# Kernel optimization log

Hardware: AMD Instinct MI355X
Metric: run time of the kernel (lower is better)

## Reference

```python
import jax, jax.numpy as jnp
import numpy as np

# blueprint: (root_input_idx, children) where child >= 0 -> input[child], child < 0 -> hidden[-child-1]
BLUEPRINT = [(0, [0, 1, 2, 3]), (4, [4, 5, 6, 7]), (8, [8, 9, 10, 11]), (12, [12, 13, 14, 15]), (0, [-1, -2, -3, -4])]
B, T, V, E, H, TAGS = 32768, 16, 32000, 32, 64, 64


def setup_inputs() -> dict:
    key = jax.random.key(0)
    ks = jax.random.split(key, 13)
    x = jax.random.randint(ks[0], (B, T), 0, V)  # token ids (never hit pad row V)
    s = jax.random.randint(ks[1], (B,), 1, 5)    # lengths in [1, 4]
    sc = 0.125  # ~1/sqrt(H), matches torch LSTM uniform init scale
    emb = (jax.random.normal(ks[2], (V + 1, E), dtype=jnp.float32) * 0.1).at[V].set(0.0)
    Wih = jax.random.uniform(ks[3], (4 * H, E), minval=-sc, maxval=sc, dtype=jnp.float32)
    Whh = jax.random.uniform(ks[4], (4 * H, H), minval=-sc, maxval=sc, dtype=jnp.float32)
    bih = jax.random.uniform(ks[5], (4 * H,), minval=-sc, maxval=sc, dtype=jnp.float32)
    bhh = jax.random.uniform(ks[6], (4 * H,), minval=-sc, maxval=sc, dtype=jnp.float32)
    h0 = jax.random.uniform(ks[7], (H,), minval=-1.0, maxval=1.0, dtype=jnp.float32)
    c0 = jax.random.uniform(ks[8], (H,), minval=-1.0, maxval=1.0, dtype=jnp.float32)
    Wc = jax.random.uniform(ks[9], (E, H + E), minval=-0.1, maxval=0.1, dtype=jnp.float32)
    bc = jnp.zeros((E,), dtype=jnp.float32)
    Wt = jax.random.uniform(ks[10], (TAGS, E), minval=-0.18, maxval=0.18, dtype=jnp.float32)
    bt = jnp.zeros((TAGS,), dtype=jnp.float32)
    return {"x": x, "s": s, "emb": emb, "Wih": Wih, "Whh": Whh, "bih": bih, "bhh": bhh,
            "h0": h0, "c0": c0, "Wc": Wc, "bc": bc, "Wt": Wt, "bt": bt}


def _lstm_seq(cseq, h0b, c0b, Wih, Whh, b):
    # cseq: [B, L, E] -> outputs [B, L, H]; torch gate order i, f, g, o
    def step(carry, xt):
        h, cc = carry
        g = xt @ Wih.T + h @ Whh.T + b
        i, f, gg, o = jnp.split(g, 4, axis=-1)
        cc = jax.nn.sigmoid(f) * cc + jax.nn.sigmoid(i) * jnp.tanh(gg)
        h = jax.nn.sigmoid(o) * jnp.tanh(cc)
        return (h, cc), h
    _, hs = jax.lax.scan(step, (h0b, c0b), jnp.swapaxes(cseq, 0, 1))
    return jnp.swapaxes(hs, 0, 1)


def reference(x, s, emb, Wih, Whh, bih, bhh, h0, c0, Wc, bc, Wt, bt):
    bsz = x.shape[0]
    inputs = emb[x]  # [B, T, E]
    h0b = jnp.broadcast_to(h0[None, :], (bsz, h0.shape[0]))
    c0b = jnp.broadcast_to(c0[None, :], (bsz, c0.shape[0]))
    b = bih + bhh
    hidden = []
    for root, children in BLUEPRINT:
        r = inputs[:, root]  # [B, E]
        ch = [inputs[:, c] if c >= 0 else hidden[-c - 1] for c in children]
        cseq = jnp.stack(ch, axis=1)  # [B, L, E]
        L = cseq.shape[1]
        o = _lstm_seq(cseq, h0b, c0b, Wih, Whh, b)  # [B, L, H]
        # pack/pad semantics: positions t >= s[b] are zero after pad_packed; relu(0)=0
        mask = (jnp.arange(L)[None, :] < s[:, None]).astype(o.dtype)
        o = jax.nn.relu(o) * mask[..., None]
        last = o[:, -1]  # [B, H] (zero where s[b] < L, matching torch)
        comb = jax.nn.relu(jnp.concatenate([r, last], axis=1) @ Wc.T + bc)  # [B, E]
        hidden.append(comb)
    logits = hidden[-1] @ Wt.T + bt  # [B, TAGS]
    return jax.nn.log_softmax(logits, axis=1)
```

## Files before the change

kernel.cpp:

```cpp
#include <hip/hip_runtime.h>

#define NB 32768
#define NT 16
#define NV 32001
#define NE 32
#define NTAGS 64

typedef __attribute__((ext_vector_type(8))) short short8;
typedef __attribute__((ext_vector_type(4))) float f4;

#define MFMA16(a, b, c) __builtin_amdgcn_mfma_f32_16x16x32_bf16(a, b, c, 0, 0, 0)
#define CFENCE() asm volatile("" ::: "memory")
#define LDSSYNC() asm volatile("s_waitcnt lgkmcnt(0)" ::: "memory")

__device__ __forceinline__ float sigm_(float x) {
    return __builtin_amdgcn_rcpf(1.0f + __expf(-x));
}
__device__ __forceinline__ float tanh2_(float x) {
    float e = __expf(-2.0f * x);
    return fmaf(2.0f, __builtin_amdgcn_rcpf(1.0f + e), -1.0f);
}
__device__ __forceinline__ short f2bf(float x) {
    union { float f; unsigned u; } v; v.f = x;
    unsigned r = v.u + 0x7fffu + ((v.u >> 16) & 1u);
    return (short)(r >> 16);
}

__global__ __launch_bounds__(1024) void classify_prep(
    const int* __restrict__ s, const float* __restrict__ emb,
    const float* __restrict__ Wih, const float* __restrict__ Whh,
    const float* __restrict__ bih, const float* __restrict__ bhh,
    const float* __restrict__ Wc, const float* __restrict__ Wt,
    short* __restrict__ embH, short* __restrict__ wpack, short* __restrict__ wc1,
    short* __restrict__ wc2, short* __restrict__ wth, float* __restrict__ bsum,
    int* __restrict__ cH, int* __restrict__ listH, int* __restrict__ listL) {
    __shared__ int wbH[16], wbL[16];
    const int tid = threadIdx.x, b = blockIdx.x;
    if (b < 32) {
        const int row = b * 1024 + tid;
        const bool heavy = s[row] >= 4;
        unsigned long long mk = __ballot(heavy);
        const int wv = tid >> 6, ln = tid & 63;
        if (ln == 0) wbH[wv] = __popcll(mk);
        __syncthreads();
        if (tid == 0) {
            int tH = 0, tL = 0;
#pragma unroll
            for (int i = 0; i < 16; ++i) {
                int ch = wbH[i];
                wbH[i] = tH; wbL[i] = tL;
                tH += ch; tL += 64 - ch;
            }
            cH[b] = tH;
        }
        __syncthreads();
        unsigned long long ltm = (1ull << ln) - 1ull;
        if (heavy) listH[b * 1024 + wbH[wv] + __popcll(mk & ltm)] = row;
        else       listL[b * 1024 + wbL[wv] + __popcll((~mk) & ltm)] = row;
    }
    for (int i = b * 1024 + tid; i < NV * NE; i += 262144) embH[i] = f2bf(emb[i]);
    if (b == 32) {
        for (int t = tid; t < 18432; t += 1024) {
            int r = t / 72, c = t % 72;
            wpack[t] = f2bf(c < 64 ? Whh[r * 64 + c] : 0.f);
        }
        for (int t = tid; t < 10240; t += 1024) {
            int r = t / 40, c = t % 40;
            wpack[18432 + t] = f2bf(c < 32 ? Wih[r * 32 + c] : 0.f);
        }
        if (tid < 1024) { int r = tid >> 5, c = tid & 31; wc1[tid] = f2bf(Wc[r * 96 + c]); }
        for (int t = tid; t < 2048; t += 1024) {
            int r = t >> 6, c = t & 63;
            wc2[t] = f2bf(Wc[r * 96 + 32 + c]);
        }
        for (int t = tid; t < 2048; t += 1024) {
            int r = t >> 5, c = t & 31;
            wth[t] = f2bf(Wt[r * 32 + c]);
        }
        if (tid < 256) bsum[tid] = bih[tid] + bhh[tid];
    }
}

__global__ __launch_bounds__(256, 2) void main_fused(
    const int* __restrict__ x, const float* __restrict__ emb,
    const float* __restrict__ h0, const float* __restrict__ c0,
    const float* __restrict__ Wc, const float* __restrict__ bc,
    const float* __restrict__ Wt, const float* __restrict__ bt,
    const float* __restrict__ bsum,
    const short* __restrict__ wpack, const short* __restrict__ wc1,
    const short* __restrict__ wc2, const short* __restrict__ wth,
    const short* __restrict__ embH, const int* __restrict__ cH,
    const int* __restrict__ listH, const int* __restrict__ listL,
    float* __restrict__ out) {
    __shared__ __align__(16) short sWhh[18432];
    __shared__ __align__(16) short sHA[4][16 * 72];
    __shared__ __align__(16) short sCmb[4][16 * 40];
    __shared__ __align__(16) short sC4[4][4 * 40];

    const int tid = threadIdx.x, wave = tid >> 6, lane = tid & 63;
    const int q = lane >> 4, n = lane & 15;
    const int NW = gridDim.x * 4;
    const int gw = blockIdx.x * 4 + wave;

    int cs = (lane < 32) ? cH[lane] : 0;
    int v = cs;
#pragma unroll
    for (int o = 1; o < 32; o <<= 1) { int t2 = __shfl_up(v, o); if (lane >= o) v += t2; }
    const int vIncl = v, vExcl = v - cs;
    const int nH = __shfl(vIncl, 31);
    const int nL = NB - nH;
    const int liIncl = (lane + 1) * 1024 - vIncl;
    const int liExcl = lane * 1024 - vExcl;
    const int nHW = (nH + 3) >> 2;

    if ((int)blockIdx.x * 4 < nHW) {
        for (int i = tid; i < 2304; i += 256)
            ((uint4*)sWhh)[i] = ((const uint4*)wpack)[i];
        __syncthreads();
    }

    if (gw < nHW) {
        short* hA = sHA[wave];
        short* cmb = sCmb[wave];
        short* c4 = sC4[wave];
        const short* wihG = wpack + 18432;

        short8 wihR[16];
#pragma unroll
        for (int tl = 0; tl < 16; ++tl)
            wihR[tl] = *(const short8*)&wihG[(tl * 16 + n) * 40 + q * 8];

        float bias16[16];
#pragma unroll
        for (int tl = 0; tl < 16; ++tl) bias16[tl] = bsum[tl * 16 + n];
        float bc2[2] = {bc[n], bc[16 + n]};
        float bt4[4] = {bt[n], bt[16 + n], bt[32 + n], bt[48 + n]};
        float c0v[4]; short h0b[4];
#pragma unroll
        for (int u = 0; u < 4; ++u) { c0v[u] = c0[u * 16 + n]; h0b[u] = f2bf(h0[u * 16 + n]); }

        const f4 zero4 = {0.f, 0.f, 0.f, 0.f};
        f4 acc[16];
        float cst[4][4];

        auto initSt = [&]() {
#pragma unroll
            for (int u = 0; u < 4; ++u) {
                short hb = h0b[u];
#pragma unroll
                for (int r = 0; r < 4; ++r) {
                    cst[r][u] = c0v[u];
                    hA[(q * 4 + r) * 72 + u * 16 + n] = hb;
                }
            }
            CFENCE();
        };
        auto doStep = [&](short8 aP, bool doRelu) {
            short8 ah0 = *(const short8*)&hA[n * 72 + q * 8];
            short8 ah1 = *(const short8*)&hA[n * 72 + 32 + q * 8];
#pragma unroll
            for (int tl = 0; tl < 16; ++tl) acc[tl] = MFMA16(aP, wihR[tl], zero4);
#pragma unroll
            for (int tl = 0; tl < 16; ++tl) {
                const short* rbp = &sWhh[(tl * 16 + n) * 72 + q * 8];
                f4 t0 = acc[tl];
                t0 = MFMA16(ah0, *(const short8*)rbp, t0);
                t0 = MFMA16(ah1, *(const short8*)(rbp + 32), t0);
                acc[tl] = t0;
            }
            CFENCE();
#pragma unroll
            for (int u = 0; u < 4; ++u)
#pragma unroll
                for (int r = 0; r < 4; ++r) {
                    float ip = acc[u][r] + bias16[u];
                    float fp = acc[4 + u][r] + bias16[4 + u];
                    float gp = acc[8 + u][r] + bias16[8 + u];
                    float op = acc[12 + u][r] + bias16[12 + u];
                    float cc = fmaf(sigm_(fp), cst[r][u], sigm_(ip) * tanh2_(gp));
                    cst[r][u] = cc;
                    float hh = sigm_(op) * tanh2_(cc);
                    if (doRelu) hh = fmaxf(hh, 0.f);
                    hA[(q * 4 + r) * 72 + u * 16 + n] = f2bf(hh);
                }
            CFENCE();
        };
        auto combMM = [&](short8 aroot, short* dst, int strideSel) {
            short8 lh0 = *(const short8*)&hA[n * 72 + q * 8];
            short8 lh1 = *(const short8*)&hA[n * 72 + 32 + q * 8];
#pragma unroll
            for (int tl2 = 0; tl2 < 2; ++tl2) {
                float bv = bc2[tl2];
                f4 t0 = {bv, bv, bv, bv};
                short8 b1 = *(const short8*)&wc1[(tl2 * 16 + n) * 32 + q * 8];
                t0 = MFMA16(aroot, b1, t0);
                const short* rbp = &wc2[(tl2 * 16 + n) * 64 + q * 8];
                t0 = MFMA16(lh0, *(const short8*)rbp, t0);
                t0 = MFMA16(lh1, *(const short8*)(rbp + 32), t0);
#pragma unroll
                for (int r = 0; r < 4; ++r) {
                    int ui = strideSel ? (q * 4 + r) : r;
                    dst[ui * 40 + tl2 * 16 + n] = f2bf(fmaxf(t0[r], 0.f));
                }
            }
            CFENCE();
        };

#pragma unroll 1
        for (int it = gw; it * 4 < nH; it += NW) {
            const int base = it * 4;
            int idxq = min(base + q, nH - 1);
            int sl = 0;
#pragma unroll
            for (int b2 = 0; b2 < 32; ++b2) sl += (__shfl(vIncl, b2) <= idxq) ? 1 : 0;
            const int row = listH[sl * 1024 + idxq - __shfl(vExcl, sl)];
            const int tokAll = x[row * 16 + n];
            const int liBase = (n & 3) * 16 + (n >> 2) * 4;

            initSt();
            int tok = __shfl(tokAll, liBase);
            short8 aNext = *(const short8*)&embH[tok * 32 + q * 8];
            const short8 aRoot = aNext;
#pragma unroll 1
            for (int t = 0; t < 4; ++t) {
                short8 aP = aNext;
                if (t < 3) {
                    int tk2 = __shfl(tokAll, liBase + t + 1);
                    aNext = *(const short8*)&embH[tk2 * 32 + q * 8];
                }
                doStep(aP, t == 3);
            }
            combMM(aRoot, cmb, 1);

            initSt();
            int tokR = __shfl(tokAll, (n & 3) * 16);
            short8 aR4 = *(const short8*)&embH[tokR * 32 + q * 8];
#pragma unroll 1
            for (int t = 0; t < 4; ++t) {
                short8 aC = *(const short8*)&cmb[(t * 4 + (n & 3)) * 40 + q * 8];
                doStep(aC, t == 3);
            }
            combMM(aR4, c4, 0);

            short8 cA = *(const short8*)&c4[(n & 3) * 40 + q * 8];
            f4 a3[4];
#pragma unroll
            for (int tl3 = 0; tl3 < 4; ++tl3) {
                float bv = bt4[tl3];
                f4 t0 = {bv, bv, bv, bv};
                short8 bW = *(const short8*)&wth[(tl3 * 16 + n) * 32 + q * 8];
                a3[tl3] = MFMA16(cA, bW, t0);
            }
#pragma unroll
            for (int r = 0; r < 4; ++r) {
                float l0 = a3[0][r], l1 = a3[1][r], l2 = a3[2][r], l3 = a3[3][r];
                float mx = fmaxf(fmaxf(l0, l1), fmaxf(l2, l3));
#pragma unroll
                for (int o2 = 8; o2; o2 >>= 1) mx = fmaxf(mx, __shfl_xor(mx, o2));
                float sm = __expf(l0 - mx) + __expf(l1 - mx) +
                           __expf(l2 - mx) + __expf(l3 - mx);
#pragma unroll
                for (int o2 = 8; o2; o2 >>= 1) sm += __shfl_xor(sm, o2);
                float lse = mx + __logf(sm);
                if (q == r && base + r < nH) {
                    out[row * 64 + n] = l0 - lse;
                    out[row * 64 + 16 + n] = l1 - lse;
                    out[row * 64 + 32 + n] = l2 - lse;
                    out[row * 64 + 48 + n] = l3 - lse;
                }
            }
        }
    }

    if (nL > 0) {
        short* cmbL = sCmb[wave];
        f4 bcV[2], btV[4];
#pragma unroll
        for (int t = 0; t < 2; ++t) { float bv = bc[t * 16 + n]; bcV[t] = f4{bv, bv, bv, bv}; }
#pragma unroll
        for (int t = 0; t < 4; ++t) { float bv = bt[t * 16 + n]; btV[t] = f4{bv, bv, bv, bv}; }
        const int lgw = NW - 1 - gw;
#pragma unroll 1
        for (int base = lgw * 16; base < nL; base += NW * 16) {
            int idx = min(base + lane, nL - 1);
            int sl = 0;
#pragma unroll
            for (int b2 = 0; b2 < 32; ++b2) sl += (__shfl(liIncl, b2) <= idx) ? 1 : 0;
            const int lrow = listL[sl * 1024 + idx - __shfl(liExcl, sl)];
            const int ltok = x[lrow * 16];
            short8 aE = *(const short8*)&embH[__shfl(ltok, n) * 32 + q * 8];
#pragma unroll
            for (int tl2 = 0; tl2 < 2; ++tl2) {
                short8 b1 = *(const short8*)&wc1[(tl2 * 16 + n) * 32 + q * 8];
                f4 t0 = MFMA16(aE, b1, bcV[tl2]);
#pragma unroll
                for (int r = 0; r < 4; ++r)
                    cmbL[(q * 4 + r) * 40 + tl2 * 16 + n] = f2bf(fmaxf(t0[r], 0.f));
            }
            CFENCE();
            short8 cA = *(const short8*)&cmbL[n * 40 + q * 8];
            f4 a3[4];
#pragma unroll
            for (int tl3 = 0; tl3 < 4; ++tl3) {
                short8 bW = *(const short8*)&wth[(tl3 * 16 + n) * 32 + q * 8];
                a3[tl3] = MFMA16(cA, bW, btV[tl3]);
            }
#pragma unroll
            for (int r = 0; r < 4; ++r) {
                float l0 = a3[0][r], l1 = a3[1][r], l2 = a3[2][r], l3 = a3[3][r];
                float mx = fmaxf(fmaxf(l0, l1), fmaxf(l2, l3));
#pragma unroll
                for (int o2 = 8; o2; o2 >>= 1) mx = fmaxf(mx, __shfl_xor(mx, o2));
                float sm = __expf(l0 - mx) + __expf(l1 - mx) +
                           __expf(l2 - mx) + __expf(l3 - mx);
#pragma unroll
                for (int o2 = 8; o2; o2 >>= 1) sm += __shfl_xor(sm, o2);
                float lse = mx + __logf(sm);
                int rowO = __shfl(lrow, q * 4 + r);
                if (base + q * 4 + r < nL) {
                    out[rowO * 64 + n] = l0 - lse;
                    out[rowO * 64 + 16 + n] = l1 - lse;
                    out[rowO * 64 + 32 + n] = l2 - lse;
                    out[rowO * 64 + 48 + n] = l3 - lse;
                }
            }
            CFENCE();
        }
    }
}

__global__ __launch_bounds__(512) void tagger_fallback(
    const int* __restrict__ x, const int* __restrict__ s, const float* __restrict__ emb,
    const float* __restrict__ Wih, const float* __restrict__ Whh,
    const float* __restrict__ bih, const float* __restrict__ bhh,
    const float* __restrict__ h0, const float* __restrict__ c0,
    const float* __restrict__ Wc, const float* __restrict__ bc,
    const float* __restrict__ Wt, const float* __restrict__ bt,
    float* __restrict__ out) {
    __shared__ float4 WhhP[4096];
    __shared__ float combBuf[8][128];
    for (int i = threadIdx.x; i < 4096; i += 512) {
        int k = i & 63, jj = i >> 6;
        WhhP[k * 64 + jj] = make_float4(Whh[jj * 64 + k], Whh[(jj + 64) * 64 + k],
                                        Whh[(jj + 128) * 64 + k], Whh[(jj + 192) * 64 + k]);
    }
    __syncthreads();
    const int wave = threadIdx.x >> 6, j = threadIdx.x & 63, jm = j & 31;
    const int b = blockIdx.x * 8 + wave;
    const int sv = s[b];
    const int* xb = x + b * NT;
    const float bcj = bc[jm];
    auto rc_val = [&](int tok) -> float {
        float r = 0.f;
#pragma unroll
        for (int k = 0; k < 32; ++k) r = fmaf(emb[tok * NE + k], Wc[jm * 96 + k], r);
        return r;
    };
    float comb4;
    if (sv >= 4) {
        const float h0j = h0[j], c0j = c0[j];
        float4 bsj = make_float4(bih[j] + bhh[j], bih[j + 64] + bhh[j + 64],
                                 bih[j + 128] + bhh[j + 128], bih[j + 192] + bhh[j + 192]);
#pragma unroll 1
        for (int node = 0; node < 4; ++node) {
            float h = h0j, c = c0j;
#pragma unroll 1
            for (int t = 0; t < 4; ++t) {
                int tok = xb[node * 4 + t];
                float4 p = bsj;
#pragma unroll
                for (int k = 0; k < 32; ++k) {
                    float e = emb[tok * NE + k];
                    p.x = fmaf(e, Wih[j * 32 + k], p.x);
                    p.y = fmaf(e, Wih[(j + 64) * 32 + k], p.y);
                    p.z = fmaf(e, Wih[(j + 128) * 32 + k], p.z);
                    p.w = fmaf(e, Wih[(j + 192) * 32 + k], p.w);
                }
                float4 a = make_float4(0.f, 0.f, 0.f, 0.f);
#pragma unroll
                for (int k = 0; k < 64; ++k) {
                    float hk = __shfl(h, k);
                    float4 w = WhhP[k * 64 + j];
                    a.x = fmaf(hk, w.x, a.x); a.y = fmaf(hk, w.y, a.y);
                    a.z = fmaf(hk, w.z, a.z); a.w = fmaf(hk, w.w, a.w);
                }
                a.x += p.x; a.y += p.y; a.z += p.z; a.w += p.w;
                float ig = sigm_(a.x), fg = sigm_(a.y), gg = tanh2_(a.z), og = sigm_(a.w);
                c = fmaf(fg, c, ig * gg);
                h = og * tanh2_(c);
            }
            float last = fmaxf(h, 0.f);
            float acc = rc_val(xb[node * 4]) + bcj;
#pragma unroll
            for (int k = 0; k < 64; ++k)
                acc = fmaf(__shfl(last, k), Wc[jm * 96 + 32 + k], acc);
            if (j < 32) combBuf[wave][node * 32 + j] = fmaxf(acc, 0.f);
        }
        LDSSYNC();
        float h = h0j, c = c0j;
#pragma unroll 1
        for (int t = 0; t < 4; ++t) {
            float4 a = make_float4(0.f, 0.f, 0.f, 0.f);
#pragma unroll
            for (int k = 0; k < 32; ++k) {
                float ck = combBuf[wave][t * 32 + k];
                a.x = fmaf(ck, Wih[j * 32 + k], a.x);
                a.y = fmaf(ck, Wih[(j + 64) * 32 + k], a.y);
                a.z = fmaf(ck, Wih[(j + 128) * 32 + k], a.z);
                a.w = fmaf(ck, Wih[(j + 192) * 32 + k], a.w);
            }
#pragma unroll
            for (int k = 0; k < 64; ++k) {
                float hk = __shfl(h, k);
                float4 w = WhhP[k * 64 + j];
                a.x = fmaf(hk, w.x, a.x); a.y = fmaf(hk, w.y, a.y);
                a.z = fmaf(hk, w.z, a.z); a.w = fmaf(hk, w.w, a.w);
            }
            a.x += bih[j] + bhh[j]; a.y += bih[j + 64] + bhh[j + 64];
            a.z += bih[j + 128] + bhh[j + 128]; a.w += bih[j + 192] + bhh[j + 192];
            float ig = sigm_(a.x), fg = sigm_(a.y), gg = tanh2_(a.z), og = sigm_(a.w);
            c = fmaf(fg, c, ig * gg);
            h = og * tanh2_(c);
        }
        float last = fmaxf(h, 0.f);
        float acc = rc_val(xb[0]) + bcj;
#pragma unroll
        for (int k = 0; k < 64; ++k)
            acc = fmaf(__shfl(last, k), Wc[jm * 96 + 32 + k], acc);
        comb4 = fmaxf(acc, 0.f);
    } else {
        comb4 = fmaxf(rc_val(xb[0]) + bcj, 0.f);
    }
    float logit = bt[j];
    const float* wtr = Wt + j * 32;
#pragma unroll
    for (int k = 0; k < 32; ++k) logit = fmaf(__shfl(comb4, k), wtr[k], logit);
    float mx = logit;
#pragma unroll
    for (int off = 32; off; off >>= 1) mx = fmaxf(mx, __shfl_xor(mx, off));
    float ex = __expf(logit - mx);
    float sum = ex;
#pragma unroll
    for (int off = 32; off; off >>= 1) sum += __shfl_xor(sum, off);
    out[b * 64 + j] = logit - mx - __logf(sum);
}

extern "C" void kernel_launch(void* const* d_in, const int* in_sizes, int n_in,
                              void* d_out, int out_size, void* d_ws, size_t ws_size,
                              hipStream_t stream) {
    const int* x = (const int*)d_in[0];
    const int* s = (const int*)d_in[1];
    const float* emb = (const float*)d_in[2];
    const float* Wih = (const float*)d_in[3];
    const float* Whh = (const float*)d_in[4];
    const float* bih = (const float*)d_in[5];
    const float* bhh = (const float*)d_in[6];
    const float* h0 = (const float*)d_in[7];
    const float* c0 = (const float*)d_in[8];
    const float* Wc = (const float*)d_in[9];
    const float* bc = (const float*)d_in[10];
    const float* Wt = (const float*)d_in[11];
    const float* bt = (const float*)d_in[12];
    float* out = (float*)d_out;

    auto al16 = [](size_t v) { return (v + 15) & ~(size_t)15; };
    size_t off = 0;
    size_t oWpack = off; off = al16(off + (size_t)28672 * 2);
    size_t oWc1 = off;   off = al16(off + 1024 * 2);
    size_t oWc2 = off;   off = al16(off + 2048 * 2);
    size_t oWt = off;    off = al16(off + 2048 * 2);
    size_t oBsum = off;  off = al16(off + 256 * 4);
    size_t oEmbH = off;  off = al16(off + (size_t)NV * NE * 2);
    size_t oCH = off;    off = al16(off + 32 * 4);
    size_t oListH = off; off = al16(off + (size_t)NB * 4);
    size_t oListL = off; off = al16(off + (size_t)NB * 4);
    size_t need = off;

    char* ws = (char*)d_ws;
    if (ws_size >= need) {
        short* wpack = (short*)(ws + oWpack);
        short* wc1 = (short*)(ws + oWc1);
        short* wc2 = (short*)(ws + oWc2);
        short* wth = (short*)(ws + oWt);
        float* bsum = (float*)(ws + oBsum);
        short* embH = (short*)(ws + oEmbH);
        int* cHp = (int*)(ws + oCH);
        int* listH = (int*)(ws + oListH);
        int* listL = (int*)(ws + oListL);

        classify_prep<<<dim3(256), dim3(1024), 0, stream>>>(
            s, emb, Wih, Whh, bih, bhh, Wc, Wt,
            embH, wpack, wc1, wc2, wth, bsum, cHp, listH, listL);
        main_fused<<<dim3(768), dim3(256), 0, stream>>>(
            x, emb, h0, c0, Wc, bc, Wt, bt, bsum,
            wpack, wc1, wc2, wth, embH, cHp, listH, listL, out);
    } else {
        tagger_fallback<<<dim3(4096), dim3(512), 0, stream>>>(
            x, s, emb, Wih, Whh, bih, bhh, h0, c0, Wc, bc, Wt, bt, out);
    }
}
```

Measured before the change: 151.2 us.

## Share top-level LSTM across block waves by splitting gates per wave

Heavy rows are now handled per block in groups of 16 instead of per wave in groups of 4. The final-level LSTM over the four combined children is batched across the whole block, with each wave computing one 16-unit gate slice and exchanging hidden state through shared memory under block barriers. This removes the redundant 4x-padded top-level recurrence, in which only 4 of 16 MFMA rows were useful. Light rows are handed to dedicated non-heavy blocks when available, and h0 fragments are kept in registers rather than rewritten to LDS. The cost is added __syncthreads per step, which could stall waves, and a different load split between heavy and light blocks.

```diff
diff --git a/kernel.cpp b/kernel.cpp
--- a/kernel.cpp
+++ b/kernel.cpp
@@ -96,6 +96,7 @@
     __shared__ __align__(16) short sHA[4][16 * 72];
     __shared__ __align__(16) short sCmb[4][16 * 40];
     __shared__ __align__(16) short sC4[4][4 * 40];
+    __shared__ int sRow[16];
 
     const int tid = threadIdx.x, wave = tid >> 6, lane = tid & 63;
     const int q = lane >> 4, n = lane & 15;
@@ -111,18 +112,19 @@
     const int nL = NB - nH;
     const int liIncl = (lane + 1) * 1024 - vIncl;
     const int liExcl = lane * 1024 - vExcl;
-    const int nHW = (nH + 3) >> 2;
-
-    if ((int)blockIdx.x * 4 < nHW) {
+    const int nHB = (nH + 15) >> 4;
+    const bool heavyBlk = (int)blockIdx.x < nHB;
+
+    if (heavyBlk) {
         for (int i = tid; i < 2304; i += 256)
             ((uint4*)sWhh)[i] = ((const uint4*)wpack)[i];
         __syncthreads();
     }
 
-    if (gw < nHW) {
+    if (heavyBlk) {
         short* hA = sHA[wave];
-        short* cmb = sCmb[wave];
-        short* c4 = sC4[wave];
+        short* cmbB = sCmb[0];
+        short* c4 = sC4[0];
         const short* wihG = wpack + 18432;
 
         short8 wihR[16];
@@ -135,29 +137,22 @@
         for (int tl = 0; tl < 16; ++tl) bias16[tl] = bsum[tl * 16 + n];
         float bc2[2] = {bc[n], bc[16 + n]};
         float bt4[4] = {bt[n], bt[16 + n], bt[32 + n], bt[48 + n]};
-        float c0v[4]; short h0b[4];
-#pragma unroll
-        for (int u = 0; u < 4; ++u) { c0v[u] = c0[u * 16 + n]; h0b[u] = f2bf(h0[u * 16 + n]); }
+        float c0v[4];
+#pragma unroll
+        for (int u = 0; u < 4; ++u) c0v[u] = c0[u * 16 + n];
+        short8 h0f0, h0f1;
+#pragma unroll
+        for (int j = 0; j < 8; ++j) {
+            h0f0[j] = f2bf(h0[q * 8 + j]);
+            h0f1[j] = f2bf(h0[32 + q * 8 + j]);
+        }
+        const float c0w = c0[wave * 16 + n];
 
         const f4 zero4 = {0.f, 0.f, 0.f, 0.f};
         f4 acc[16];
         float cst[4][4];
 
-        auto initSt = [&]() {
-#pragma unroll
-            for (int u = 0; u < 4; ++u) {
-                short hb = h0b[u];
-#pragma unroll
-                for (int r = 0; r < 4; ++r) {
-                    cst[r][u] = c0v[u];
-                    hA[(q * 4 + r) * 72 + u * 16 + n] = hb;
-                }
-            }
-            CFENCE();
-        };
-        auto doStep = [&](short8 aP, bool doRelu) {
-            short8 ah0 = *(const short8*)&hA[n * 72 + q * 8];
-            short8 ah1 = *(const short8*)&hA[n * 72 + 32 + q * 8];
+        auto doStep = [&](short8 aP, short8 ah0, short8 ah1, bool doRelu) {
 #pragma unroll
             for (int tl = 0; tl < 16; ++tl) acc[tl] = MFMA16(aP, wihR[tl], zero4);
 #pragma unroll
@@ -185,42 +180,27 @@
                 }
             CFENCE();
         };
-        auto combMM = [&](short8 aroot, short* dst, int strideSel) {
-            short8 lh0 = *(const short8*)&hA[n * 72 + q * 8];
-            short8 lh1 = *(const short8*)&hA[n * 72 + 32 + q * 8];
-#pragma unroll
-            for (int tl2 = 0; tl2 < 2; ++tl2) {
-                float bv = bc2[tl2];
-                f4 t0 = {bv, bv, bv, bv};
-                short8 b1 = *(const short8*)&wc1[(tl2 * 16 + n) * 32 + q * 8];
-                t0 = MFMA16(aroot, b1, t0);
-                const short* rbp = &wc2[(tl2 * 16 + n) * 64 + q * 8];
-                t0 = MFMA16(lh0, *(const short8*)rbp, t0);
-                t0 = MFMA16(lh1, *(const short8*)(rbp + 32), t0);
-#pragma unroll
-                for (int r = 0; r < 4; ++r) {
-                    int ui = strideSel ? (q * 4 + r) : r;
-                    dst[ui * 40 + tl2 * 16 + n] = f2bf(fmaxf(t0[r], 0.f));
-                }
-            }
-            CFENCE();
-        };
 
 #pragma unroll 1
-        for (int it = gw; it * 4 < nH; it += NW) {
-            const int base = it * 4;
-            int idxq = min(base + q, nH - 1);
+        for (int itb = blockIdx.x; itb * 16 < nH; itb += (int)gridDim.x) {
+            const int base = itb * 16;
+            int idxq = min(base + wave * 4 + q, nH - 1);
             int sl = 0;
 #pragma unroll
             for (int b2 = 0; b2 < 32; ++b2) sl += (__shfl(vIncl, b2) <= idxq) ? 1 : 0;
             const int row = listH[sl * 1024 + idxq - __shfl(vExcl, sl)];
+            if (n == 0) sRow[wave * 4 + q] = row;
             const int tokAll = x[row * 16 + n];
             const int liBase = (n & 3) * 16 + (n >> 2) * 4;
 
-            initSt();
+#pragma unroll
+            for (int u = 0; u < 4; ++u)
+#pragma unroll
+                for (int r = 0; r < 4; ++r) cst[r][u] = c0v[u];
             int tok = __shfl(tokAll, liBase);
             short8 aNext = *(const short8*)&embH[tok * 32 + q * 8];
             const short8 aRoot = aNext;
+            short8 a0 = h0f0, a1 = h0f1;
 #pragma unroll 1
             for (int t = 0; t < 4; ++t) {
                 short8 aP = aNext;
@@ -228,103 +208,203 @@
                     int tk2 = __shfl(tokAll, liBase + t + 1);
                     aNext = *(const short8*)&embH[tk2 * 32 + q * 8];
                 }
-                doStep(aP, t == 3);
-            }
-            combMM(aRoot, cmb, 1);
-
-            initSt();
-            int tokR = __shfl(tokAll, (n & 3) * 16);
-            short8 aR4 = *(const short8*)&embH[tokR * 32 + q * 8];
+                doStep(aP, a0, a1, t == 3);
+                if (t < 3) {
+                    a0 = *(const short8*)&hA[n * 72 + q * 8];
+                    a1 = *(const short8*)&hA[n * 72 + 32 + q * 8];
+                }
+            }
+            {
+                short8 lh0 = *(const short8*)&hA[n * 72 + q * 8];
+                short8 lh1 = *(const short8*)&hA[n * 72 + 32 + q * 8];
+#pragma unroll
+                for (int tl2 = 0; tl2 < 2; ++tl2) {
+                    float bv = bc2[tl2];
+                    f4 t0 = {bv, bv, bv, bv};
+                    short8 b1 = *(const short8*)&wc1[(tl2 * 16 + n) * 32 + q * 8];
+                    t0 = MFMA16(aRoot, b1, t0);
+                    const short* rbp = &wc2[(tl2 * 16 + n) * 64 + q * 8];
+                    t0 = MFMA16(lh0, *(const short8*)rbp, t0);
+                    t0 = MFMA16(lh1, *(const short8*)(rbp + 32), t0);
+#pragma unroll
+                    for (int r = 0; r < 4; ++r) {
+                        int m = q * 4 + r;
+                        cmbB[((m >> 2) * 16 + wave * 4 + (m & 3)) * 40 + tl2 * 16 + n] =
+                            f2bf(fmaxf(t0[r], 0.f));
+                    }
+                }
+            }
+            __syncthreads();
+
+            float bias4[4];
+            short8 wih4[4];
+#pragma unroll
+            for (int j = 0; j < 4; ++j) {
+                bias4[j] = bsum[(j * 4 + wave) * 16 + n];
+                wih4[j] = *(const short8*)&wihG[((j * 4 + wave) * 16 + n) * 40 + q * 8];
+            }
+            short8 aCs0 = *(const short8*)&cmbB[(0 * 16 + n) * 40 + q * 8];
+            short8 aCs1 = *(const short8*)&cmbB[(1 * 16 + n) * 40 + q * 8];
+            short8 aCs2 = *(const short8*)&cmbB[(2 * 16 + n) * 40 + q * 8];
+            short8 aCs3 = *(const short8*)&cmbB[(3 * 16 + n) * 40 + q * 8];
+            float cstw[4] = {c0w, c0w, c0w, c0w};
+            short8 b0 = h0f0, b1 = h0f1;
+            f4 ac4[4];
+#pragma unroll
+            for (int t = 0; t < 4; ++t) {
+                short* hbw = (t & 1) ? sHA[1] : sHA[0];
+                short8 aC = (t == 0) ? aCs0 : (t == 1) ? aCs1 : (t == 2) ? aCs2 : aCs3;
+#pragma unroll
+                for (int j = 0; j < 4; ++j) ac4[j] = MFMA16(aC, wih4[j], zero4);
+#pragma unroll
+                for (int j = 0; j < 4; ++j) {
+                    const short* rbp = &sWhh[((j * 4 + wave) * 16 + n) * 72 + q * 8];
+                    f4 t0 = ac4[j];
+                    t0 = MFMA16(b0, *(const short8*)rbp, t0);
+                    t0 = MFMA16(b1, *(const short8*)(rbp + 32), t0);
+                    ac4[j] = t0;
+                }
+                CFENCE();
+#pragma unroll
+                for (int r = 0; r < 4; ++r) {
+                    float ip = ac4[0][r] + bias4[0];
+                    float fp = ac4[1][r] + bias4[1];
+                    float gp = ac4[2][r] + bias4[2];
+                    float op = ac4[3][r] + bias4[3];
+                    float cc = fmaf(sigm_(fp), cstw[r], sigm_(ip) * tanh2_(gp));
+                    cstw[r] = cc;
+                    float hh = sigm_(op) * tanh2_(cc);
+                    if (t == 3) hh = fmaxf(hh, 0.f);
+                    hbw[(q * 4 + r) * 72 + wave * 16 + n] = f2bf(hh);
+                }
+                CFENCE();
+                __syncthreads();
+                if (t < 3) {
+                    b0 = *(const short8*)&hbw[n * 72 + q * 8];
+                    b1 = *(const short8*)&hbw[n * 72 + 32 + q * 8];
+                }
+            }
+
+            {
+                const short* hL = sHA[1];
+                int rv = sRow[n];
+                int tokR = x[rv * 16];
+                short8 aR = *(const short8*)&embH[tokR * 32 + q * 8];
+                short8 lb0 = *(const short8*)&hL[n * 72 + q * 8];
+                short8 lb1 = *(const short8*)&hL[n * 72 + 32 + q * 8];
+#pragma unroll
+                for (int tl2 = 0; tl2 < 2; ++tl2) {
+                    float bv = bc2[tl2];
+                    f4 t0 = {bv, bv, bv, bv};
+                    short8 b1f = *(const short8*)&wc1[(tl2 * 16 + n) * 32 + q * 8];
+                    t0 = MFMA16(aR, b1f, t0);
+                    const short* rbp = &wc2[(tl2 * 16 + n) * 64 + q * 8];
+                    t0 = MFMA16(lb0, *(const short8*)rbp, t0);
+                    t0 = MFMA16(lb1, *(const short8*)(rbp + 32), t0);
+                    if (q == wave) {
+#pragma unroll
+                        for (int r = 0; r < 4; ++r)
+                            c4[(wave * 4 + r) * 40 + tl2 * 16 + n] = f2bf(fmaxf(t0[r], 0.f));
+                    }
+                }
+            }
+            __syncthreads();
+
+            {
+                short8 cA = *(const short8*)&c4[n * 40 + q * 8];
+                f4 a3[4];
+#pragma unroll
+                for (int tl3 = 0; tl3 < 4; ++tl3) {
+                    float bv = bt4[tl3];
+                    f4 t0 = {bv, bv, bv, bv};
+                    short8 bW = *(const short8*)&wth[(tl3 * 16 + n) * 32 + q * 8];
+                    a3[tl3] = MFMA16(cA, bW, t0);
+                }
+#pragma unroll
+                for (int r = 0; r < 4; ++r) {
+                    float l0 = a3[0][r], l1 = a3[1][r], l2 = a3[2][r], l3 = a3[3][r];
+                    float mx = fmaxf(fmaxf(l0, l1), fmaxf(l2, l3));
+#pragma unroll
+                    for (int o2 = 8; o2; o2 >>= 1) mx = fmaxf(mx, __shfl_xor(mx, o2));
+                    float sm = __expf(l0 - mx) + __expf(l1 - mx) +
+                               __expf(l2 - mx) + __expf(l3 - mx);
+#pragma unroll
+                    for (int o2 = 8; o2; o2 >>= 1) sm += __shfl_xor(sm, o2);
+                    float lse = mx + __logf(sm);
+                    if (q == wave && base + wave * 4 + r < nH) {
+                        int ro = sRow[wave * 4 + r];
+                        out[ro * 64 + n] = l0 - lse;
+                        out[ro * 64 + 16 + n] = l1 - lse;
+                        out[ro * 64 + 32 + n] = l2 - lse;
+                        out[ro * 64 + 48 + n] = l3 - lse;
+                    }
+                }
+            }
+        }
+    }
+
+    if (nL > 0) {
+        const int nLB = max((int)gridDim.x - nHB, 0);
+        int lw, nlw;
+        if (nLB > 0) {
+            if (heavyBlk) { lw = -1; nlw = 0; }
+            else { lw = ((int)blockIdx.x - nHB) * 4 + wave; nlw = nLB * 4; }
+        } else {
+            lw = NW - 1 - gw; nlw = NW;
+        }
+        if (lw >= 0) {
+            short* cmbL = sCmb[wave];
+            f4 bcV[2], btV[4];
+#pragma unroll
+            for (int t = 0; t < 2; ++t) { float bv = bc[t * 16 + n]; bcV[t] = f4{bv, bv, bv, bv}; }
+#pragma unroll
+            for (int t = 0; t < 4; ++t) { float bv = bt[t * 16 + n]; btV[t] = f4{bv, bv, bv, bv}; }
 #pragma unroll 1
-            for (int t = 0; t < 4; ++t) {
-                short8 aC = *(const short8*)&cmb[(t * 4 + (n & 3)) * 40 + q * 8];
-                doStep(aC, t == 3);
-            }
-            combMM(aR4, c4, 0);
-
-            short8 cA = *(const short8*)&c4[(n & 3) * 40 + q * 8];
-            f4 a3[4];
-#pragma unroll
-            for (int tl3 = 0; tl3 < 4; ++tl3) {
-                float bv = bt4[tl3];
-                f4 t0 = {bv, bv, bv, bv};
-                short8 bW = *(const short8*)&wth[(tl3 * 16 + n) * 32 + q * 8];
-                a3[tl3] = MFMA16(cA, bW, t0);
-            }
-#pragma unroll
-            for (int r = 0; r < 4; ++r) {
-                float l0 = a3[0][r], l1 = a3[1][r], l2 = a3[2][r], l3 = a3[3][r];
-                float mx = fmaxf(fmaxf(l0, l1), fmaxf(l2, l3));
-#pragma unroll
-                for (int o2 = 8; o2; o2 >>= 1) mx = fmaxf(mx, __shfl_xor(mx, o2));
-                float sm = __expf(l0 - mx) + __expf(l1 - mx) +
-                           __expf(l2 - mx) + __expf(l3 - mx);
-#pragma unroll
-                for (int o2 = 8; o2; o2 >>= 1) sm += __shfl_xor(sm, o2);
-                float lse = mx + __logf(sm);
-                if (q == r && base + r < nH) {
-                    out[row * 64 + n] = l0 - lse;
-                    out[row * 64 + 16 + n] = l1 - lse;
-                    out[row * 64 + 32 + n] = l2 - lse;
-                    out[row * 64 + 48 + n] = l3 - lse;
-                }
-            }
-        }
-    }
-
-    if (nL > 0) {
-        short* cmbL = sCmb[wave];
-        f4 bcV[2], btV[4];
-#pragma unroll
-        for (int t = 0; t < 2; ++t) { float bv = bc[t * 16 + n]; bcV[t] = f4{bv, bv, bv, bv}; }
-#pragma unroll
-        for (int t = 0; t < 4; ++t) { float bv = bt[t * 16 + n]; btV[t] = f4{bv, bv, bv, bv}; }
-        const int lgw = NW - 1 - gw;
-#pragma unroll 1
-        for (int base = lgw * 16; base < nL; base += NW * 16) {
-            int idx = min(base + lane, nL - 1);
-            int sl = 0;
-#pragma unroll
-            for (int b2 = 0; b2 < 32; ++b2) sl += (__shfl(liIncl, b2) <= idx) ? 1 : 0;
-            const int lrow = listL[sl * 1024 + idx - __shfl(liExcl, sl)];
-            const int ltok = x[lrow * 16];
-            short8 aE = *(const short8*)&embH[__shfl(ltok, n) * 32 + q * 8];
-#pragma unroll
-            for (int tl2 = 0; tl2 < 2; ++tl2) {
-                short8 b1 = *(const short8*)&wc1[(tl2 * 16 + n) * 32 + q * 8];
-                f4 t0 = MFMA16(aE, b1, bcV[tl2]);
-#pragma unroll
-                for (int r = 0; r < 4; ++r)
-                    cmbL[(q * 4 + r) * 40 + tl2 * 16 + n] = f2bf(fmaxf(t0[r], 0.f));
-            }
-            CFENCE();
-            short8 cA = *(const short8*)&cmbL[n * 40 + q * 8];
-            f4 a3[4];
-#pragma unroll
-            for (int tl3 = 0; tl3 < 4; ++tl3) {
-                short8 bW = *(const short8*)&wth[(tl3 * 16 + n) * 32 + q * 8];
-                a3[tl3] = MFMA16(cA, bW, btV[tl3]);
-            }
-#pragma unroll
-            for (int r = 0; r < 4; ++r) {
-                float l0 = a3[0][r], l1 = a3[1][r], l2 = a3[2][r], l3 = a3[3][r];
-                float mx = fmaxf(fmaxf(l0, l1), fmaxf(l2, l3));
-#pragma unroll
-                for (int o2 = 8; o2; o2 >>= 1) mx = fmaxf(mx, __shfl_xor(mx, o2));
-                float sm = __expf(l0 - mx) + __expf(l1 - mx) +
-                           __expf(l2 - mx) + __expf(l3 - mx);
-#pragma unroll
-                for (int o2 = 8; o2; o2 >>= 1) sm += __shfl_xor(sm, o2);
-                float lse = mx + __logf(sm);
-                int rowO = __shfl(lrow, q * 4 + r);
-                if (base + q * 4 + r < nL) {
-                    out[rowO * 64 + n] = l0 - lse;
-                    out[rowO * 64 + 16 + n] = l1 - lse;
-                    out[rowO * 64 + 32 + n] = l2 - lse;
-                    out[rowO * 64 + 48 + n] = l3 - lse;
-                }
-            }
-            CFENCE();
+            for (int base = lw * 16; base < nL; base += nlw * 16) {
+                int idx = min(base + lane, nL - 1);
+                int sl = 0;
+#pragma unroll
+                for (int b2 = 0; b2 < 32; ++b2) sl += (__shfl(liIncl, b2) <= idx) ? 1 : 0;
+                const int lrow = listL[sl * 1024 + idx - __shfl(liExcl, sl)];
+                const int ltok = x[lrow * 16];
+                short8 aE = *(const short8*)&embH[__shfl(ltok, n) * 32 + q * 8];
+#pragma unroll
+                for (int tl2 = 0; tl2 < 2; ++tl2) {
+                    short8 b1 = *(const short8*)&wc1[(tl2 * 16 + n) * 32 + q * 8];
+                    f4 t0 = MFMA16(aE, b1, bcV[tl2]);
+#pragma unroll
+                    for (int r = 0; r < 4; ++r)
+                        cmbL[(q * 4 + r) * 40 + tl2 * 16 + n] = f2bf(fmaxf(t0[r], 0.f));
+                }
+                CFENCE();
+                short8 cA = *(const short8*)&cmbL[n * 40 + q * 8];
+                f4 a3[4];
+#pragma unroll
+                for (int tl3 = 0; tl3 < 4; ++tl3) {
+                    short8 bW = *(const short8*)&wth[(tl3 * 16 + n) * 32 + q * 8];
+                    a3[tl3] = MFMA16(cA, bW, btV[tl3]);
+                }
+#pragma unroll
+                for (int r = 0; r < 4; ++r) {
+                    float l0 = a3[0][r], l1 = a3[1][r], l2 = a3[2][r], l3 = a3[3][r];
+                    float mx = fmaxf(fmaxf(l0, l1), fmaxf(l2, l3));
+#pragma unroll
+                    for (int o2 = 8; o2; o2 >>= 1) mx = fmaxf(mx, __shfl_xor(mx, o2));
+                    float sm = __expf(l0 - mx) + __expf(l1 - mx) +
+                               __expf(l2 - mx) + __expf(l3 - mx);
+#pragma unroll
+                    for (int o2 = 8; o2; o2 >>= 1) sm += __shfl_xor(sm, o2);
+                    float lse = mx + __logf(sm);
+                    int rowO = __shfl(lrow, q * 4 + r);
+                    if (base + q * 4 + r < nL) {
+                        out[rowO * 64 + n] = l0 - lse;
+                        out[rowO * 64 + 16 + n] = l1 - lse;
+                        out[rowO * 64 + 32 + n] = l2 - lse;
+                        out[rowO * 64 + 48 + n] = l3 - lse;
+                    }
+                }
+                CFENCE();
+            }
         }
     }
 }
```

New measurement: 145.4 us. 3.8% less time.
